# Kernel optimization log

Hardware: AMD Instinct MI355X
Metric: run time of the kernel (lower is better)

## Reference

```python
import jax, jax.numpy as jnp
import numpy as np

B, S, F_IN, D, DFF, MEM, L, H = 32, 512, 64, 512, 2048, 1024, 3, 8
K_NEIGH = 3
TEMP = 1.0


def _pos_encoding(s, d):
    pos = np.arange(s, dtype=np.float64)[:, None]
    div = np.exp(np.arange(0, d, 2, dtype=np.float64) * (-np.log(10000.0) / d))
    pe = np.zeros((s, d), np.float32)
    pe[:, 0::2] = np.sin(pos * div)
    pe[:, 1::2] = np.cos(pos * div)
    return jnp.asarray(pe)


def _ln(x, g, b, eps=1e-5):
    m = x.mean(-1, keepdims=True)
    v = ((x - m) ** 2).mean(-1, keepdims=True)
    return (x - m) * jax.lax.rsqrt(v + eps) * g + b


def _mha(x, qkv_w, qkv_b, out_w, out_b):
    b, s, d = x.shape
    dh = d // H
    qkv = x @ qkv_w.T + qkv_b                      # (b,s,3d)
    q, k, v = jnp.split(qkv, 3, axis=-1)
    rs = lambda t: t.reshape(b, s, H, dh).transpose(0, 2, 1, 3)   # (b,h,s,dh)
    q, k, v = rs(q), rs(k), rs(v)
    scores = jnp.einsum('bhqd,bhkd->bhqk', q, k) / np.sqrt(dh).astype(np.float32)
    att = jax.nn.softmax(scores, axis=-1)
    o = jnp.einsum('bhqk,bhkd->bhqd', att, v).transpose(0, 2, 1, 3).reshape(b, s, d)
    return o @ out_w.T + out_b


def _construct_graph(x):
    # x: (B, S, F) -> adjacency (B, F, F) via kNN on rank-1 similarity (as in source)
    f = x.mean(axis=1)                                   # (B,F)
    n = jnp.linalg.norm(f, axis=1, keepdims=True)
    fn = f / jnp.maximum(n, 1e-12)                       # F.normalize over full vector
    sim = jnp.einsum('bi,bj->bij', fn, fn)               # (B,F,F)
    nf = f.shape[1]
    k = min(K_NEIGH, nf - 1)
    _, idx = jax.lax.top_k(sim, k + 1)                   # (B,F,k+1)
    idx = idx[..., 1:]                                   # drop top-1 (self under source's assumption)
    bidx = jnp.arange(f.shape[0])[:, None, None]
    ridx = jnp.arange(nf)[None, :, None]
    A = jnp.zeros((f.shape[0], nf, nf), x.dtype).at[bidx, ridx, idx].set(1.0)
    A = jnp.maximum(A, jnp.swapaxes(A, 1, 2))            # symmetrize
    di = jnp.arange(nf)
    return A.at[:, di, di].set(1.0)                      # fill_diagonal_(1)


def _gcn(x, A, w1, b1, w2, b2):
    deg = A.sum(2, keepdims=True)
    An = A / jnp.where(deg == 0, jnp.ones_like(deg), deg)
    xt = jnp.swapaxes(x, 1, 2)                           # (B,F,S)
    h = jax.nn.relu(jnp.einsum('bfg,bgh->bfh', An, xt @ w1.T + b1))
    h = jnp.einsum('bfg,bgh->bfh', An, h @ w2.T + b2)
    return jnp.swapaxes(h, 1, 2)                         # (B,S,F)


def _metg_forward(x, W_in, b_in, qkv_w, qkv_b, out_w, out_b, ln1_g, ln1_b,
                  ln2_g, ln2_b, ff1_w, ff1_b, ff2_w, ff2_b, memory,
                  fc1_w, fc1_b, fc2_w, fc2_b, gc1_w, gc1_b, gc2_w, gc2_b):
    # transformer branch
    h = x @ W_in.T + b_in                                # (B,S,D)
    h = h + _pos_encoding(h.shape[1], h.shape[2])
    for l in range(L):  # post-norm TransformerEncoderLayer, relu FFN, dropout=eval
        h = _ln(h + _mha(h, qkv_w[l], qkv_b[l], out_w[l], out_b[l]), ln1_g[l], ln1_b[l])
        ff = jax.nn.relu(h @ ff1_w[l].T + ff1_b[l]) @ ff2_w[l].T + ff2_b[l]
        h = _ln(h + ff, ln2_g[l], ln2_b[l])
    # memory module
    sims = (h @ memory.T) / TEMP                         # (B,S,MEM)
    attn = jax.nn.softmax(sims, axis=-1)
    upd = attn @ memory                                  # (B,S,D)
    # decoder
    cat = jnp.concatenate([h, upd], axis=-1)             # (B,S,2D)
    t_out = jax.nn.relu(cat @ fc1_w.T + fc1_b) @ fc2_w.T + fc2_b
    # GCN branch
    A = _construct_graph(x)
    g_out = _gcn(x, A, gc1_w, gc1_b, gc2_w, gc2_b)
    return t_out, g_out, attn


def setup_inputs() -> dict:
    key = jax.random.key(0)
    ks = jax.random.split(key, 12)
    w = lambda k, shape, s=0.02: jax.random.normal(k, shape, jnp.float32) * s
    return {
        'x': jax.random.normal(ks[0], (B, S, F_IN), jnp.float32),
        'W_in': w(ks[1], (D, F_IN)), 'b_in': jnp.zeros((D,), jnp.float32),
        'qkv_w': w(ks[2], (L, 3 * D, D)), 'qkv_b': jnp.zeros((L, 3 * D), jnp.float32),
        'out_w': w(ks[3], (L, D, D)), 'out_b': jnp.zeros((L, D), jnp.float32),
        'ln1_g': jnp.ones((L, D), jnp.float32), 'ln1_b': jnp.zeros((L, D), jnp.float32),
        'ln2_g': jnp.ones((L, D), jnp.float32), 'ln2_b': jnp.zeros((L, D), jnp.float32),
        'ff1_w': w(ks[4], (L, DFF, D)), 'ff1_b': jnp.zeros((L, DFF), jnp.float32),
        'ff2_w': w(ks[5], (L, D, DFF)), 'ff2_b': jnp.zeros((L, D), jnp.float32),
        'memory': w(ks[6], (MEM, D), 0.05),
        'fc1_w': w(ks[7], (D, 2 * D)), 'fc1_b': jnp.zeros((D,), jnp.float32),
        'fc2_w': w(ks[8], (F_IN, D)), 'fc2_b': jnp.zeros((F_IN,), jnp.float32),
        'gc1_w': w(ks[9], (D, S)), 'gc1_b': jnp.zeros((D,), jnp.float32),
        'gc2_w': w(ks[10], (S, D)), 'gc2_b': jnp.zeros((S,), jnp.float32),
    }


def reference(x, W_in, b_in, qkv_w, qkv_b, out_w, out_b, ln1_g, ln1_b,
              ln2_g, ln2_b, ff1_w, ff1_b, ff2_w, ff2_b, memory,
              fc1_w, fc1_b, fc2_w, fc2_b, gc1_w, gc1_b, gc2_w, gc2_b):
    return _metg_forward(x, W_in, b_in, qkv_w, qkv_b, out_w, out_b, ln1_g, ln1_b,
                         ln2_g, ln2_b, ff1_w, ff1_b, ff2_w, ff2_b, memory,
                         fc1_w, fc1_b, fc2_w, fc2_b, gc1_w, gc1_b, gc2_w, gc2_b)
```

## Files before the change

kernel.cpp:

```cpp
#include <hip/hip_runtime.h>
#include <hip/hip_bf16.h>
#include <math.h>


namespace {

typedef unsigned short ushort_t;
using bf16x8 = __attribute__((ext_vector_type(8))) __bf16;
using f32x4 = __attribute__((ext_vector_type(4))) float;
using ushort8 = __attribute__((ext_vector_type(8))) unsigned short;

constexpr int Mrows = 32 * 512;
constexpr size_t MB = 1048576;

__device__ __forceinline__ unsigned short f2bf(float f) {
  unsigned int u = __builtin_bit_cast(unsigned int, f);
  u += 0x7fffu + ((u >> 16) & 1u);
  return (unsigned short)(u >> 16);
}
__device__ __forceinline__ float bf2f(ushort_t u) {
  unsigned int v = ((unsigned int)u) << 16;
  return __builtin_bit_cast(float, v);
}

__device__ __forceinline__ void g2lds16(const void* g, void* l) {
  __builtin_amdgcn_global_load_lds(
      (const __attribute__((address_space(1))) unsigned int*)g,
      (__attribute__((address_space(3))) unsigned int*)l, 16, 0, 0);
}

template <bool RELU, bool BF16OUT>
__global__ __launch_bounds__(512, 2) void gemm256(const ushort_t* __restrict__ A,
                                                  const ushort_t* __restrict__ B,
                                                  const float* __restrict__ bias,
                                                  void* __restrict__ Cv,
                                                  int K, int lda, int ldc) {
  __shared__ __align__(16) ushort_t As[2][256 * 64];
  __shared__ __align__(16) ushort_t Bs[2][256 * 64];
  const int t = threadIdx.x;
  const int w = t >> 6, l = t & 63;
  const int m0 = blockIdx.x << 8, n0 = blockIdx.y << 8;
  const int srow8 = l >> 3;
  const int scol = ((l & 7) ^ srow8) << 3;
  const ushort_t* agp = A + (size_t)(m0 + w * 32 + srow8) * lda + scol;
  const ushort_t* bgp = B + (size_t)(n0 + w * 32 + srow8) * K + scol;
  const int wr = w >> 2, wcn = w & 3;
  const int lr = l & 15, g = l >> 4;
  const int sw = (l & 7) << 4;
  const int nt = K >> 6;
  f32x4 acc[8][4] = {};
#pragma unroll
  for (int i = 0; i < 4; ++i) {
    g2lds16(agp + (size_t)(i * 8) * lda, &As[0][(w * 32 + i * 8) * 64]);
    g2lds16(bgp + (size_t)(i * 8) * K, &Bs[0][(w * 32 + i * 8) * 64]);
  }
#pragma unroll
  for (int i = 0; i < 4; ++i) {
    g2lds16(agp + (size_t)(i * 8) * lda + 64, &As[1][(w * 32 + i * 8) * 64]);
    g2lds16(bgp + (size_t)(i * 8) * K + 64, &Bs[1][(w * 32 + i * 8) * 64]);
  }
  for (int j = 0; j < nt; ++j) {
    const int c = j & 1;
    asm volatile("s_waitcnt vmcnt(8)" ::: "memory");
    __builtin_amdgcn_s_barrier();
    asm volatile("" ::: "memory");
    const char* abase = (const char*)&As[c][0];
    const char* bbase = (const char*)&Bs[c][0];
#pragma unroll
    for (int ki = 0; ki < 2; ++ki) {
      const int kb = (ki * 64 + g * 16) ^ sw;
      bf16x8 af[8], bfr[4];
#pragma unroll
      for (int mi = 0; mi < 8; ++mi)
        af[mi] = *(const bf16x8*)(abase + (wr * 128 + mi * 16 + lr) * 128 + kb);
#pragma unroll
      for (int ni = 0; ni < 4; ++ni)
        bfr[ni] = *(const bf16x8*)(bbase + (wcn * 64 + ni * 16 + lr) * 128 + kb);
      __builtin_amdgcn_s_setprio(1);
#pragma unroll
      for (int mi = 0; mi < 8; ++mi)
#pragma unroll
        for (int ni = 0; ni < 4; ++ni)
          acc[mi][ni] = __builtin_amdgcn_mfma_f32_16x16x32_bf16(af[mi], bfr[ni],
                                                                acc[mi][ni], 0, 0, 0);
      __builtin_amdgcn_s_setprio(0);
    }
    asm volatile("s_waitcnt lgkmcnt(0)" ::: "memory");
    __builtin_amdgcn_s_barrier();
    asm volatile("" ::: "memory");
    if (j + 2 < nt) {
      const size_t ko = (size_t)(j + 2) * 64;
#pragma unroll
      for (int i = 0; i < 4; ++i) {
        g2lds16(agp + (size_t)(i * 8) * lda + ko, &As[c][(w * 32 + i * 8) * 64]);
        g2lds16(bgp + (size_t)(i * 8) * K + ko, &Bs[c][(w * 32 + i * 8) * 64]);
      }
    }
  }
  float bb[4];
#pragma unroll
  for (int ni = 0; ni < 4; ++ni) {
    const int ci = n0 + wcn * 64 + ni * 16 + lr;
    bb[ni] = bias ? bias[ci] : 0.f;
  }
  const int crow0 = m0 + wr * 128 + g * 4;
#pragma unroll
  for (int mi = 0; mi < 8; ++mi)
#pragma unroll
    for (int ni = 0; ni < 4; ++ni) {
      const int ci = n0 + wcn * 64 + ni * 16 + lr;
#pragma unroll
      for (int v = 0; v < 4; ++v) {
        float val = acc[mi][ni][v] + bb[ni];
        if (RELU) val = fmaxf(val, 0.f);
        const size_t off = (size_t)(crow0 + mi * 16 + v) * ldc + ci;
        if (BF16OUT) ((ushort_t*)Cv)[off] = f2bf(val);
        else         ((float*)Cv)[off] = val;
      }
    }
}

template <bool RELU, bool BF16OUT>
__global__ __launch_bounds__(256) void gemm_bf16(const ushort_t* __restrict__ A,
                                                 const ushort_t* __restrict__ B,
                                                 const float* __restrict__ bias,
                                                 void* __restrict__ Cv,
                                                 int K, int lda, int ldc, int Nclip) {
  __shared__ __align__(16) ushort_t As[128 * 64];
  __shared__ __align__(16) ushort_t Bs[128 * 64];
  const int t = threadIdx.x;
  const int w = t >> 6, l = t & 63;
  const int m0 = blockIdx.x << 7, n0 = blockIdx.y << 7;
  const int srow8 = l >> 3;
  const int scol = ((l & 7) ^ srow8) << 3;
  const ushort_t* agp = A + (size_t)(m0 + w * 32 + srow8) * lda + scol;
  const ushort_t* bgp = B + (size_t)(n0 + w * 32 + srow8) * K + scol;
  ushort_t* alds = &As[(w * 32) * 64];
  ushort_t* blds = &Bs[(w * 32) * 64];
  const int wr = w >> 1, wc = w & 1;
  const int lr = l & 15, g = l >> 4;
  const int sw = (l & 7) << 4;
  f32x4 acc[4][4] = {};
  for (int kt = 0; kt < K; kt += 64) {
    __syncthreads();
#pragma unroll
    for (int i = 0; i < 4; ++i) {
      g2lds16(agp + (size_t)(i * 8) * lda + kt, alds + i * 8 * 64);
      g2lds16(bgp + (size_t)(i * 8) * K + kt, blds + i * 8 * 64);
    }
    __syncthreads();
#pragma unroll
    for (int ki = 0; ki < 2; ++ki) {
      bf16x8 af[4], bf[4];
      const int kb = (ki * 64 + g * 16) ^ sw;
#pragma unroll
      for (int mi = 0; mi < 4; ++mi)
        af[mi] = *(const bf16x8*)((const char*)As + (wr * 64 + mi * 16 + lr) * 128 + kb);
#pragma unroll
      for (int ni = 0; ni < 4; ++ni)
        bf[ni] = *(const bf16x8*)((const char*)Bs + (wc * 64 + ni * 16 + lr) * 128 + kb);
#pragma unroll
      for (int mi = 0; mi < 4; ++mi)
#pragma unroll
        for (int ni = 0; ni < 4; ++ni)
          acc[mi][ni] = __builtin_amdgcn_mfma_f32_16x16x32_bf16(af[mi], bf[ni],
                                                                acc[mi][ni], 0, 0, 0);
    }
  }
  float bb[4];
#pragma unroll
  for (int ni = 0; ni < 4; ++ni) {
    const int ci = n0 + wc * 64 + ni * 16 + lr;
    bb[ni] = (bias && ci < Nclip) ? bias[ci] : 0.f;
  }
  const int crow0 = m0 + wr * 64 + g * 4;
#pragma unroll
  for (int mi = 0; mi < 4; ++mi)
#pragma unroll
    for (int ni = 0; ni < 4; ++ni) {
      const int ci = n0 + wc * 64 + ni * 16 + lr;
      if (ci >= Nclip) continue;
#pragma unroll
      for (int v = 0; v < 4; ++v) {
        float val = acc[mi][ni][v] + bb[ni];
        if (RELU) val = fmaxf(val, 0.f);
        const size_t off = (size_t)(crow0 + mi * 16 + v) * ldc + ci;
        if (BF16OUT) ((ushort_t*)Cv)[off] = f2bf(val);
        else         ((float*)Cv)[off] = val;
      }
    }
}

__global__ __launch_bounds__(256) void flash_attn_mfma(const ushort_t* __restrict__ qkvb,
                                                       ushort_t* __restrict__ ctxb) {
  __shared__ __align__(16) ushort_t Qs[64 * 64];
  __shared__ __align__(16) ushort_t Ks[64 * 64];
  __shared__ __align__(16) ushort_t VT[64 * 64];
  __shared__ __align__(16) ushort_t Ps[64 * 64];
  const int qb = blockIdx.x, hh = blockIdx.y, b = blockIdx.z;
  const int t = threadIdx.x, w = t >> 6, l = t & 63;
  const int g = l >> 4, lr = l & 15, l7 = l & 7;
  const ushort_t* qkv0 = qkvb + (size_t)b * 512 * 1536 + hh * 64;
  {
    const int r8 = l >> 3;
    const int gcol = (l7 ^ r8) << 3;
#pragma unroll
    for (int i = 0; i < 2; ++i) {
      const int row = w * 16 + i * 8 + r8;
      g2lds16(qkv0 + (size_t)(qb * 64 + row) * 1536 + gcol, &Qs[(w * 16 + i * 8) * 64]);
    }
  }
  float mst = -INFINITY, lst = 0.f;
  f32x4 oacc[4] = {};
  const int vk0 = (t & 31) * 2;
  const int vdh0 = (t >> 5) * 8;
  for (int kt = 0; kt < 8; ++kt) {
    __syncthreads();
    {
      const int r8 = l >> 3;
      const int gcol = (l7 ^ r8) << 3;
#pragma unroll
      for (int i = 0; i < 2; ++i) {
        const int row = w * 16 + i * 8 + r8;
        g2lds16(qkv0 + 512 + (size_t)(kt * 64 + row) * 1536 + gcol,
                &Ks[(w * 16 + i * 8) * 64]);
      }
    }
    {
      const ushort_t* vp = qkv0 + 1024 + (size_t)(kt * 64 + vk0) * 1536 + vdh0;
      ushort8 v0 = *(const ushort8*)vp;
      ushort8 v1 = *(const ushort8*)(vp + 1536);
      const int slotbase = vk0 >> 3;
      const int inb = (vk0 & 7) * 2;
#pragma unroll
      for (int e = 0; e < 8; ++e) {
        const int dh = vdh0 + e;
        unsigned int word = (unsigned int)v0[e] | ((unsigned int)v1[e] << 16);
        *(unsigned int*)((char*)VT + dh * 128 + (((slotbase ^ (dh & 7)) << 4) + inb)) = word;
      }
    }
    __syncthreads();
    f32x4 sacc[4] = {};
#pragma unroll
    for (int ki = 0; ki < 2; ++ki) {
      const int sb = ((ki * 4 + g) ^ l7) << 4;
      bf16x8 qf = *(const bf16x8*)((const char*)Qs + (w * 16 + lr) * 128 + sb);
#pragma unroll
      for (int mi = 0; mi < 4; ++mi) {
        bf16x8 kf = *(const bf16x8*)((const char*)Ks + (mi * 16 + lr) * 128 + sb);
        sacc[mi] = __builtin_amdgcn_mfma_f32_16x16x32_bf16(kf, qf, sacc[mi], 0, 0, 0);
      }
    }
    float p[4][4];
    float cmax = -INFINITY;
#pragma unroll
    for (int mi = 0; mi < 4; ++mi)
#pragma unroll
      for (int v = 0; v < 4; ++v) {
        p[mi][v] = sacc[mi][v] * 0.125f;
        cmax = fmaxf(cmax, p[mi][v]);
      }
    cmax = fmaxf(cmax, __shfl_xor(cmax, 16));
    cmax = fmaxf(cmax, __shfl_xor(cmax, 32));
    const float mnew = fmaxf(mst, cmax);
    const float al = __expf(mst - mnew);
    float csum = 0.f;
#pragma unroll
    for (int mi = 0; mi < 4; ++mi)
#pragma unroll
      for (int v = 0; v < 4; ++v) {
        p[mi][v] = __expf(p[mi][v] - mnew);
        csum += p[mi][v];
      }
    csum += __shfl_xor(csum, 16);
    csum += __shfl_xor(csum, 32);
    lst = lst * al + csum;
    mst = mnew;
#pragma unroll
    for (int mi = 0; mi < 4; ++mi) oacc[mi] *= al;
    {
      char* pbase = (char*)Ps + (w * 16 + lr) * 128;
#pragma unroll
      for (int mi = 0; mi < 4; ++mi)
#pragma unroll
        for (int vp2 = 0; vp2 < 2; ++vp2) {
          const int klo = mi * 16 + g * 4 + vp2 * 2;
          unsigned int word = (unsigned int)f2bf(p[mi][vp2 * 2]) |
                              ((unsigned int)f2bf(p[mi][vp2 * 2 + 1]) << 16);
          *(unsigned int*)(pbase + (((klo >> 3) ^ l7) << 4) + (klo & 7) * 2) = word;
        }
    }
#pragma unroll
    for (int ki = 0; ki < 2; ++ki) {
      const int sb = ((ki * 4 + g) ^ l7) << 4;
      bf16x8 pf = *(const bf16x8*)((const char*)Ps + (w * 16 + lr) * 128 + sb);
#pragma unroll
      for (int mi = 0; mi < 4; ++mi) {
        bf16x8 vf = *(const bf16x8*)((const char*)VT + (mi * 16 + lr) * 128 + sb);
        oacc[mi] = __builtin_amdgcn_mfma_f32_16x16x32_bf16(vf, pf, oacc[mi], 0, 0, 0);
      }
    }
  }
  const float inv = 1.f / lst;
  ushort_t* op = ctxb + (size_t)(b * 512 + qb * 64 + w * 16 + lr) * 512 + hh * 64;
#pragma unroll
  for (int mi = 0; mi < 4; ++mi)
#pragma unroll
    for (int vp2 = 0; vp2 < 2; ++vp2) {
      const int dh = mi * 16 + g * 4 + vp2 * 2;
      unsigned int word = (unsigned int)f2bf(oacc[mi][vp2 * 2] * inv) |
                          ((unsigned int)f2bf(oacc[mi][vp2 * 2 + 1] * inv) << 16);
      *(unsigned int*)(op + dh) = word;
    }
}

#define OUTER16(ACC, A4, B4) do { \
  ACC[0][0] += (A4).x*(B4).x; ACC[0][1] += (A4).x*(B4).y; ACC[0][2] += (A4).x*(B4).z; ACC[0][3] += (A4).x*(B4).w; \
  ACC[1][0] += (A4).y*(B4).x; ACC[1][1] += (A4).y*(B4).y; ACC[1][2] += (A4).y*(B4).z; ACC[1][3] += (A4).y*(B4).w; \
  ACC[2][0] += (A4).z*(B4).x; ACC[2][1] += (A4).z*(B4).y; ACC[2][2] += (A4).z*(B4).z; ACC[2][3] += (A4).z*(B4).w; \
  ACC[3][0] += (A4).w*(B4).x; ACC[3][1] += (A4).w*(B4).y; ACC[3][2] += (A4).w*(B4).z; ACC[3][3] += (A4).w*(B4).w; \
} while (0)

__global__ __launch_bounds__(256) void win_pe_gemm(const float* __restrict__ A,
                                                   const float* __restrict__ Bm,
                                                   const float* __restrict__ bias,
                                                   const float* __restrict__ peb,
                                                   ushort_t* __restrict__ hbb) {
  __shared__ float As[16][68];
  __shared__ float Bs[16][68];
  const int t = threadIdx.x;
  const int m0 = blockIdx.x << 6;
  const int n0 = blockIdx.y << 6;
  const int r0 = (t >> 4) << 2;
  const int c0 = (t & 15) << 2;
  const int lm = t >> 2;
  const int lk4 = (t & 3) << 2;
  float acc[4][4] = {{0.f, 0.f, 0.f, 0.f}, {0.f, 0.f, 0.f, 0.f},
                     {0.f, 0.f, 0.f, 0.f}, {0.f, 0.f, 0.f, 0.f}};
  for (int kt = 0; kt < 64; kt += 16) {
    __syncthreads();
    float4 av = *reinterpret_cast<const float4*>(A + (size_t)(m0 + lm) * 64 + kt + lk4);
    As[lk4 + 0][lm] = av.x; As[lk4 + 1][lm] = av.y;
    As[lk4 + 2][lm] = av.z; As[lk4 + 3][lm] = av.w;
    float4 bv = *reinterpret_cast<const float4*>(Bm + (size_t)(n0 + lm) * 64 + kt + lk4);
    Bs[lk4 + 0][lm] = bv.x; Bs[lk4 + 1][lm] = bv.y;
    Bs[lk4 + 2][lm] = bv.z; Bs[lk4 + 3][lm] = bv.w;
    __syncthreads();
#pragma unroll
    for (int k = 0; k < 16; ++k) {
      float4 a4 = *reinterpret_cast<const float4*>(&As[k][r0]);
      float4 b4 = *reinterpret_cast<const float4*>(&Bs[k][c0]);
      OUTER16(acc, a4, b4);
    }
  }
  const float bb0 = bias[n0 + c0 + 0], bb1 = bias[n0 + c0 + 1];
  const float bb2 = bias[n0 + c0 + 2], bb3 = bias[n0 + c0 + 3];
#pragma unroll
  for (int i = 0; i < 4; ++i) {
    const int row = m0 + r0 + i;
    float4 p = *reinterpret_cast<const float4*>(peb + (size_t)(row & 511) * 512 + n0 + c0);
    ushort4 ob;
    ob.x = f2bf(acc[i][0] + bb0 + p.x);
    ob.y = f2bf(acc[i][1] + bb1 + p.y);
    ob.z = f2bf(acc[i][2] + bb2 + p.z);
    ob.w = f2bf(acc[i][3] + bb3 + p.w);
    *reinterpret_cast<ushort4*>(hbb + (size_t)row * 512 + n0 + c0) = ob;
  }
}

__global__ __launch_bounds__(256) void ln_wave(const ushort_t* __restrict__ hbi,
                                               const ushort_t* __restrict__ resb,
                                               const float* __restrict__ g,
                                               const float* __restrict__ bt,
                                               ushort_t* __restrict__ hbo, int hbs) {
  const int t = threadIdx.x;
  const size_t row = (size_t)blockIdx.x * 4 + (t >> 6);
  const int lane = t & 63;
  const size_t base = row * 512 + lane * 8;
  ushort8 hv = *reinterpret_cast<const ushort8*>(hbi + base);
  ushort8 rv = *reinterpret_cast<const ushort8*>(resb + base);
  float xs[8];
  float sum = 0.f;
#pragma unroll
  for (int i = 0; i < 8; ++i) { xs[i] = bf2f(hv[i]) + bf2f(rv[i]); sum += xs[i]; }
#pragma unroll
  for (int off = 1; off < 64; off <<= 1) sum += __shfl_xor(sum, off);
  const float mean = sum * (1.f / 512.f);
  float vs = 0.f;
#pragma unroll
  for (int i = 0; i < 8; ++i) { xs[i] -= mean; vs += xs[i] * xs[i]; }
#pragma unroll
  for (int off = 1; off < 64; off <<= 1) vs += __shfl_xor(vs, off);
  const float rstd = rsqrtf(vs * (1.f / 512.f) + 1e-5f);
  float4 g0 = *reinterpret_cast<const float4*>(g + lane * 8);
  float4 g1 = *reinterpret_cast<const float4*>(g + lane * 8 + 4);
  float4 b0 = *reinterpret_cast<const float4*>(bt + lane * 8);
  float4 b1 = *reinterpret_cast<const float4*>(bt + lane * 8 + 4);
  ushort8 o;
  o[0] = f2bf(xs[0] * rstd * g0.x + b0.x); o[1] = f2bf(xs[1] * rstd * g0.y + b0.y);
  o[2] = f2bf(xs[2] * rstd * g0.z + b0.z); o[3] = f2bf(xs[3] * rstd * g0.w + b0.w);
  o[4] = f2bf(xs[4] * rstd * g1.x + b1.x); o[5] = f2bf(xs[5] * rstd * g1.y + b1.y);
  o[6] = f2bf(xs[6] * rstd * g1.z + b1.z); o[7] = f2bf(xs[7] * rstd * g1.w + b1.w);
  *reinterpret_cast<ushort8*>(hbo + row * hbs + lane * 8) = o;
}

__global__ __launch_bounds__(256) void softmax_wave(const ushort_t* __restrict__ simsb,
                                                    float* __restrict__ attn,
                                                    ushort_t* __restrict__ attnb) {
  const int t = threadIdx.x;
  const size_t row = (size_t)blockIdx.x * 4 + (t >> 6);
  const int lane = t & 63;
  const size_t base = row * 1024 + lane * 16;
  ushort8 v0 = *reinterpret_cast<const ushort8*>(simsb + base);
  ushort8 v1 = *reinterpret_cast<const ushort8*>(simsb + base + 8);
  float xs[16];
  float mx = -INFINITY;
#pragma unroll
  for (int i = 0; i < 8; ++i) { xs[i] = bf2f(v0[i]); xs[i + 8] = bf2f(v1[i]); }
#pragma unroll
  for (int i = 0; i < 16; ++i) mx = fmaxf(mx, xs[i]);
#pragma unroll
  for (int off = 1; off < 64; off <<= 1) mx = fmaxf(mx, __shfl_xor(mx, off));
  float sum = 0.f;
#pragma unroll
  for (int i = 0; i < 16; ++i) { xs[i] = __expf(xs[i] - mx); sum += xs[i]; }
#pragma unroll
  for (int off = 1; off < 64; off <<= 1) sum += __shfl_xor(sum, off);
  const float inv = 1.f / sum;
  ushort8 o0, o1;
#pragma unroll
  for (int i = 0; i < 16; ++i) xs[i] *= inv;
#pragma unroll
  for (int i = 0; i < 4; ++i) {
    float4 f = make_float4(xs[4 * i], xs[4 * i + 1], xs[4 * i + 2], xs[4 * i + 3]);
    *reinterpret_cast<float4*>(attn + base + 4 * i) = f;
  }
#pragma unroll
  for (int i = 0; i < 8; ++i) { o0[i] = f2bf(xs[i]); o1[i] = f2bf(xs[i + 8]); }
  *reinterpret_cast<ushort8*>(attnb + base) = o0;
  *reinterpret_cast<ushort8*>(attnb + base + 8) = o1;
}

__global__ void pe_kernel(float* __restrict__ pe) {
  const int s = blockIdx.x, i = threadIdx.x;
  double div = exp((double)(2 * i) * (-log(10000.0) / 512.0));
  double a = (double)s * div;
  pe[s * 512 + 2 * i] = (float)sin(a);
  pe[s * 512 + 2 * i + 1] = (float)cos(a);
}

__global__ __launch_bounds__(256) void cvt_all(
    const float* __restrict__ qkvw, const float* __restrict__ outw,
    const float* __restrict__ ff1w, const float* __restrict__ ff2w,
    const float* __restrict__ memw, const float* __restrict__ fc1w,
    const float* __restrict__ gc1w, const float* __restrict__ gc2w,
    const float* __restrict__ fc2w,
    ushort_t* qkvb, ushort_t* outb, ushort_t* ff1b, ushort_t* ff2b,
    ushort_t* memb, ushort_t* fc1b, ushort_t* gc1b, ushort_t* gc2b,
    ushort_t* fc2p) {
  const int gidx = blockIdx.x * 256 + threadIdx.x;
  if (gidx >= 2768896) return;
  if (gidx >= 2752512) {
    const int off = gidx - 2752512;
    ushort4 o = {0, 0, 0, 0};
    if (off < 8192) {
      float4 v = reinterpret_cast<const float4*>(fc2w)[off];
      o.x = f2bf(v.x); o.y = f2bf(v.y); o.z = f2bf(v.z); o.w = f2bf(v.w);
    }
    reinterpret_cast<ushort4*>(fc2p)[off] = o;
    return;
  }
  const float* s; ushort_t* d; int off;
  if (gidx < 589824)        { s = qkvw; d = qkvb; off = gidx; }
  else if (gidx < 786432)   { s = outw; d = outb; off = gidx - 589824; }
  else if (gidx < 1572864)  { s = ff1w; d = ff1b; off = gidx - 786432; }
  else if (gidx < 2359296)  { s = ff2w; d = ff2b; off = gidx - 1572864; }
  else if (gidx < 2490368)  { s = memw; d = memb; off = gidx - 2359296; }
  else if (gidx < 2621440)  { s = fc1w; d = fc1b; off = gidx - 2490368; }
  else if (gidx < 2686976)  { s = gc1w; d = gc1b; off = gidx - 2621440; }
  else                      { s = gc2w; d = gc2b; off = gidx - 2686976; }
  float4 v = reinterpret_cast<const float4*>(s)[off];
  ushort4 o;
  o.x = f2bf(v.x); o.y = f2bf(v.y); o.z = f2bf(v.z); o.w = f2bf(v.w);
  reinterpret_cast<ushort4*>(d)[off] = o;
}

__global__ __launch_bounds__(256) void transpose_cvt(const float* __restrict__ in,
                                                     ushort_t* __restrict__ out) {
  const int g = blockIdx.x * 256 + threadIdx.x;
  const int r = g >> 9, c = g & 511;
  out[(size_t)c * 1024 + r] = f2bf(in[g]);
}

__global__ __launch_bounds__(256) void transpose_x_bf16(const float* __restrict__ x,
                                                        ushort_t* __restrict__ xtb) {
  __shared__ float Ls[64][65];
  const int sc = blockIdx.x, b = blockIdx.y;
  const int t = threadIdx.x;
  const int f = t & 63, sr = t >> 6;
#pragma unroll
  for (int j = 0; j < 16; ++j) {
    const int s = sr + 4 * j;
    Ls[s][f] = x[((size_t)(b * 512 + sc * 64 + s)) * 64 + f];
  }
  __syncthreads();
#pragma unroll
  for (int j = 0; j < 16; ++j) {
    const int fr = sr * 16 + j;
    xtb[((size_t)b * 64 + fr) * 512 + sc * 64 + f] = f2bf(Ls[f][fr]);
  }
}

__global__ __launch_bounds__(256) void fmean2(const float* __restrict__ x,
                                              float* __restrict__ fn) {
  __shared__ float part[4][64];
  const int b = blockIdx.x, t = threadIdx.x;
  const int f = t & 63, sg = t >> 6;
  float acc = 0.f;
  const float* xp = x + ((size_t)b * 512 + sg) * 64 + f;
  for (int s = sg; s < 512; s += 4, xp += 256) acc += *xp;
  part[sg][f] = acc;
  __syncthreads();
  if (t < 64) {
    float m = (part[0][t] + part[1][t] + part[2][t] + part[3][t]) * (1.f / 512.f);
    float ss = m * m;
#pragma unroll
    for (int off = 32; off; off >>= 1) ss += __shfl_xor(ss, off);
    float n = fmaxf(sqrtf(ss), 1e-12f);
    fn[b * 64 + t] = m / n;
  }
}

__global__ __launch_bounds__(256) void graph_kernel2(const float* __restrict__ fn,
                                                     float* __restrict__ An) {
  __shared__ float fv[64];
  __shared__ float Am[64][65];
  const int b = blockIdx.x, t = threadIdx.x;
  const int i = t >> 2, g = t & 3;
  if (t < 64) fv[t] = fn[b * 64 + t];
#pragma unroll
  for (int j = 0; j < 16; ++j) Am[i][g * 16 + j] = 0.f;
  __syncthreads();
  const float fi = fv[i];
  unsigned int mask = 0;
  int sel[4];
  for (int r = 0; r < 4; ++r) {
    float best = -INFINITY;
    int bi = 1 << 30;
    for (int j = 0; j < 16; ++j) {
      if (mask & (1u << j)) continue;
      float v = fi * fv[g * 16 + j];
      if (v > best) { best = v; bi = g * 16 + j; }
    }
#pragma unroll
    for (int off = 1; off < 4; off <<= 1) {
      float ov = __shfl_xor(best, off);
      int oi = __shfl_xor(bi, off);
      if (ov > best || (ov == best && oi < bi)) { best = ov; bi = oi; }
    }
    sel[r] = bi;
    if ((bi >> 4) == g) mask |= 1u << (bi & 15);
  }
  if (g == 0) { Am[i][sel[1]] = 1.f; Am[i][sel[2]] = 1.f; Am[i][sel[3]] = 1.f; }
  __syncthreads();
  float vals[16];
  float deg = 0.f;
#pragma unroll
  for (int j0 = 0; j0 < 16; ++j0) {
    const int j = g * 16 + j0;
    float v = (j == i) ? 1.f : fmaxf(Am[i][j], Am[j][i]);
    vals[j0] = v;
    deg += v;
  }
#pragma unroll
  for (int off = 1; off < 4; off <<= 1) deg += __shfl_xor(deg, off);
  const float inv = 1.f / deg;
  float* out = An + ((size_t)b * 64 + i) * 64 + g * 16;
#pragma unroll
  for (int j0 = 0; j0 < 16; ++j0) out[j0] = vals[j0] * inv;
}

template <bool RELU, bool STORE_T>
__global__ __launch_bounds__(256) void bmm_an(const float* __restrict__ An,
                                              const float* __restrict__ X,
                                              float* __restrict__ Y,
                                              ushort_t* __restrict__ Yb) {
  __shared__ float Ag[64][68];
  __shared__ float Xs[64][68];
  const int nc = blockIdx.x << 6;
  const int b = blockIdx.y;
  const int t = threadIdx.x;
  {
    const int i = t >> 2, g0 = (t & 3) << 4;
    const float* ap = An + ((size_t)b * 64 + i) * 64 + g0;
#pragma unroll
    for (int j = 0; j < 16; ++j) Ag[g0 + j][i] = ap[j];
  }
  {
    const int g = t >> 2, n4 = (t & 3) << 4;
    const float* xp = X + ((size_t)b * 64 + g) * 512 + nc + n4;
#pragma unroll
    for (int j = 0; j < 4; ++j)
      *reinterpret_cast<float4*>(&Xs[g][n4 + 4 * j]) =
          *reinterpret_cast<const float4*>(xp + 4 * j);
  }
  __syncthreads();
  const int r0 = (t >> 4) << 2, c0 = (t & 15) << 2;
  float acc[4][4] = {{0.f, 0.f, 0.f, 0.f}, {0.f, 0.f, 0.f, 0.f},
                     {0.f, 0.f, 0.f, 0.f}, {0.f, 0.f, 0.f, 0.f}};
#pragma unroll 8
  for (int g = 0; g < 64; ++g) {
    float4 a4 = *reinterpret_cast<const float4*>(&Ag[g][r0]);
    float4 x4 = *reinterpret_cast<const float4*>(&Xs[g][c0]);
    OUTER16(acc, a4, x4);
  }
  if (!STORE_T) {
#pragma unroll
    for (int i = 0; i < 4; ++i) {
      float4 o = make_float4(acc[i][0], acc[i][1], acc[i][2], acc[i][3]);
      if (RELU) {
        o.x = fmaxf(o.x, 0.f); o.y = fmaxf(o.y, 0.f);
        o.z = fmaxf(o.z, 0.f); o.w = fmaxf(o.w, 0.f);
      }
      ushort4 ob;
      ob.x = f2bf(o.x); ob.y = f2bf(o.y); ob.z = f2bf(o.z); ob.w = f2bf(o.w);
      *reinterpret_cast<ushort4*>(Yb + ((size_t)b * 64 + r0 + i) * 512 + nc + c0) = ob;
    }
  } else {
#pragma unroll
    for (int j = 0; j < 4; ++j) {
      float4 o = make_float4(acc[0][j], acc[1][j], acc[2][j], acc[3][j]);
      *reinterpret_cast<float4*>(Y + ((size_t)b * 512 + nc + c0 + j) * 64 + r0) = o;
    }
  }
}

}

extern "C" void kernel_launch(void* const* d_in, const int* in_sizes, int n_in,
                              void* d_out, int out_size, void* d_ws, size_t ws_size,
                              hipStream_t stream) {
  const float* x     = (const float*)d_in[0];
  const float* W_in  = (const float*)d_in[1];
  const float* b_in  = (const float*)d_in[2];
  const float* qkv_w = (const float*)d_in[3];
  const float* qkv_b = (const float*)d_in[4];
  const float* out_w = (const float*)d_in[5];
  const float* out_b = (const float*)d_in[6];
  const float* ln1_g = (const float*)d_in[7];
  const float* ln1_b = (const float*)d_in[8];
  const float* ln2_g = (const float*)d_in[9];
  const float* ln2_b = (const float*)d_in[10];
  const float* ff1_w = (const float*)d_in[11];
  const float* ff1_b = (const float*)d_in[12];
  const float* ff2_w = (const float*)d_in[13];
  const float* ff2_b = (const float*)d_in[14];
  const float* memw  = (const float*)d_in[15];
  const float* fc1_w = (const float*)d_in[16];
  const float* fc1_b = (const float*)d_in[17];
  const float* fc2_w = (const float*)d_in[18];
  const float* fc2_b = (const float*)d_in[19];
  const float* gc1_w = (const float*)d_in[20];
  const float* gc1_b = (const float*)d_in[21];
  const float* gc2_w = (const float*)d_in[22];
  const float* gc2_b = (const float*)d_in[23];

  char* wsb = (char*)d_ws;
  ushort_t* hb     = (ushort_t*)(wsb + 0);
  ushort_t* ctxb   = (ushort_t*)(wsb + 16 * MB);
  ushort_t* resb   = (ushort_t*)(wsb + 32 * MB);
  char*     U1     = wsb + 48 * MB;
  float*    pe     = (float*)(wsb + 144 * MB);
  ushort_t* qkv_wb = (ushort_t*)(wsb + 146 * MB);
  ushort_t* out_wb = (ushort_t*)(wsb + 151 * MB);
  ushort_t* ff1_wb = (ushort_t*)(wsb + 153 * MB);
  ushort_t* ff2_wb = (ushort_t*)(wsb + 160 * MB);
  ushort_t* mem_b  = (ushort_t*)(wsb + 166 * MB);
  ushort_t* memT_b = (ushort_t*)(wsb + 167 * MB);
  ushort_t* fc1_wb = (ushort_t*)(wsb + 168 * MB);
  ushort_t* gc1_wb = (ushort_t*)(wsb + 169 * MB);
  ushort_t* gc2_wb = (ushort_t*)(wsb + 169 * MB + 524288);
  ushort_t* fc2_wp = (ushort_t*)(wsb + 170 * MB);
  float*    fn     = (float*)(wsb + 171 * MB);
  float*    An     = (float*)(wsb + 172 * MB);

  ushort_t* qkvb    = (ushort_t*)U1;
  ushort_t* midb    = (ushort_t*)U1;
  ushort_t* catb    = (ushort_t*)U1;
  ushort_t* simsb   = (ushort_t*)(U1 + 32 * MB);
  ushort_t* attnb   = (ushort_t*)(U1 + 64 * MB);
  ushort_t* fc1outb = (ushort_t*)(U1 + 64 * MB);
  ushort_t* xtb  = (ushort_t*)U1;
  float*    t1   = (float*)(U1 + 2 * MB);
  ushort_t* h1b  = (ushort_t*)(U1 + 6 * MB);
  float*    t2   = (float*)(U1 + 8 * MB);

  float* t_out = (float*)d_out;
  float* g_out = t_out + 1048576;
  float* attn  = g_out + 1048576;

  hipLaunchKernelGGL(cvt_all, dim3(10816), dim3(256), 0, stream,
                     qkv_w, out_w, ff1_w, ff2_w, memw, fc1_w, gc1_w, gc2_w, fc2_w,
                     qkv_wb, out_wb, ff1_wb, ff2_wb, mem_b, fc1_wb, gc1_wb, gc2_wb,
                     fc2_wp);
  hipLaunchKernelGGL(transpose_cvt, dim3(2048), dim3(256), 0, stream, memw, memT_b);
  hipLaunchKernelGGL(pe_kernel, dim3(512), dim3(256), 0, stream, pe);

  hipLaunchKernelGGL(win_pe_gemm, dim3(256, 8), dim3(256), 0, stream,
                     x, W_in, b_in, pe, hb);

  for (int l = 0; l < 3; ++l) {
    hipLaunchKernelGGL((gemm256<false, true>), dim3(64, 6), dim3(512), 0, stream,
                       hb, qkv_wb + (size_t)l * 786432, qkv_b + l * 1536, qkvb,
                       512, 512, 1536);
    hipLaunchKernelGGL(flash_attn_mfma, dim3(8, 8, 32), dim3(256), 0, stream, qkvb, ctxb);
    hipLaunchKernelGGL((gemm_bf16<false, true>), dim3(128, 4), dim3(256), 0, stream,
                       ctxb, out_wb + (size_t)l * 262144, out_b + l * 512, resb,
                       512, 512, 512, 512);
    hipLaunchKernelGGL(ln_wave, dim3(Mrows / 4), dim3(256), 0, stream,
                       hb, resb, ln1_g + l * 512, ln1_b + l * 512, hb, 512);
    hipLaunchKernelGGL((gemm256<true, true>), dim3(64, 8), dim3(512), 0, stream,
                       hb, ff1_wb + (size_t)l * 1048576, ff1_b + l * 2048, midb,
                       512, 512, 2048);
    hipLaunchKernelGGL((gemm_bf16<false, true>), dim3(128, 4), dim3(256), 0, stream,
                       midb, ff2_wb + (size_t)l * 1048576, ff2_b + l * 512, resb,
                       2048, 2048, 512, 512);
    if (l < 2) {
      hipLaunchKernelGGL(ln_wave, dim3(Mrows / 4), dim3(256), 0, stream,
                         hb, resb, ln2_g + l * 512, ln2_b + l * 512, hb, 512);
    } else {
      hipLaunchKernelGGL(ln_wave, dim3(Mrows / 4), dim3(256), 0, stream,
                         hb, resb, ln2_g + l * 512, ln2_b + l * 512, catb, 1024);
    }
  }

  hipLaunchKernelGGL((gemm256<false, true>), dim3(64, 4), dim3(512), 0, stream,
                     catb, mem_b, (const float*)nullptr, simsb,
                     512, 1024, 1024);
  hipLaunchKernelGGL(softmax_wave, dim3(Mrows / 4), dim3(256), 0, stream,
                     simsb, attn, attnb);
  hipLaunchKernelGGL((gemm_bf16<false, true>), dim3(128, 4), dim3(256), 0, stream,
                     attnb, memT_b, (const float*)nullptr, catb + 512,
                     1024, 1024, 1024, 512);
  hipLaunchKernelGGL((gemm_bf16<true, true>), dim3(128, 4), dim3(256), 0, stream,
                     catb, fc1_wb, fc1_b, fc1outb, 1024, 1024, 512, 512);
  hipLaunchKernelGGL((gemm_bf16<false, false>), dim3(128, 1), dim3(256), 0, stream,
                     fc1outb, fc2_wp, fc2_b, t_out, 512, 512, 64, 64);

  hipLaunchKernelGGL(fmean2, dim3(32), dim3(256), 0, stream, x, fn);
  hipLaunchKernelGGL(graph_kernel2, dim3(32), dim3(256), 0, stream, fn, An);
  hipLaunchKernelGGL(transpose_x_bf16, dim3(8, 32), dim3(256), 0, stream, x, xtb);
  hipLaunchKernelGGL((gemm_bf16<false, false>), dim3(16, 4), dim3(256), 0, stream,
                     xtb, gc1_wb, gc1_b, t1, 512, 512, 512, 512);
  hipLaunchKernelGGL((bmm_an<true, false>), dim3(8, 32), dim3(256), 0, stream,
                     An, t1, (float*)nullptr, h1b);
  hipLaunchKernelGGL((gemm_bf16<false, false>), dim3(16, 4), dim3(256), 0, stream,
                     h1b, gc2_wb, gc2_b, t2, 512, 512, 512, 512);
  hipLaunchKernelGGL((bmm_an<false, true>), dim3(8, 32), dim3(256), 0, stream,
                     An, t2, g_out, (ushort_t*)nullptr);
}
```

Baseline: 900.9 us.

## Fuse out-proj and FF2 GEMMs with residual LayerNorm; merge graph kernels

Adds a gemm_ln kernel that computes a 64x512 full-row output tile per block, stages it in shared memory, and applies residual add plus LayerNorm before writing. This replaces the separate GEMM and ln_wave launches for both LayerNorms in each layer. The intent is to drop the resb round trip to global memory and several launches. In exchange, only 256 blocks are launched, each holding a full 512-column B tile (64KB LDS), which may lower parallelism and occupancy. It also swaps the flash attention grid order so heads vary fastest, and merges fmean2 with graph_kernel2 into a single kernel.

Result: slower. 961.7 us (+6.8%).

```diff
diff --git a/kernel.cpp b/kernel.cpp
--- a/kernel.cpp
+++ b/kernel.cpp
@@ -118,6 +118,117 @@
         else         ((float*)Cv)[off] = val;
       }
     }
+}
+
+__global__ __launch_bounds__(512, 2) void gemm_ln(const ushort_t* __restrict__ A,
+                                                  const ushort_t* __restrict__ B,
+                                                  const float* __restrict__ bias,
+                                                  const ushort_t* __restrict__ res,
+                                                  const float* __restrict__ gg,
+                                                  const float* __restrict__ bt,
+                                                  ushort_t* __restrict__ out,
+                                                  int K, int lda, int ldo) {
+  __shared__ __align__(16) char smem[8192 + 65536];
+  ushort_t* As = (ushort_t*)smem;
+  ushort_t* Bs = (ushort_t*)(smem + 8192);
+  const int t = threadIdx.x;
+  const int w = t >> 6, l = t & 63;
+  const int m0 = blockIdx.x << 6;
+  const int r8 = l >> 3;
+  const int scol = ((l & 7) ^ r8) << 3;
+  const ushort_t* agp = A + (size_t)(m0 + w * 8 + r8) * lda + scol;
+  const ushort_t* bgp = B + (size_t)(w * 64 + r8) * K + scol;
+  const int wr = w & 1, wcn = w >> 1;
+  const int lr = l & 15, gq = l >> 4;
+  const int sw = (l & 7) << 4;
+  f32x4 acc[2][8] = {};
+  for (int kt = 0; kt < K; kt += 64) {
+    __syncthreads();
+    g2lds16(agp + kt, As + (w * 8) * 64);
+#pragma unroll
+    for (int i = 0; i < 8; ++i)
+      g2lds16(bgp + (size_t)(i * 8) * K + kt, Bs + (w * 64 + i * 8) * 64);
+    __syncthreads();
+#pragma unroll
+    for (int ki = 0; ki < 2; ++ki) {
+      const int kb = (ki * 64 + gq * 16) ^ sw;
+      bf16x8 af[2], bfr[8];
+#pragma unroll
+      for (int mi = 0; mi < 2; ++mi)
+        af[mi] = *(const bf16x8*)((const char*)As + (wr * 32 + mi * 16 + lr) * 128 + kb);
+#pragma unroll
+      for (int ni = 0; ni < 8; ++ni)
+        bfr[ni] = *(const bf16x8*)((const char*)Bs + (wcn * 128 + ni * 16 + lr) * 128 + kb);
+#pragma unroll
+      for (int mi = 0; mi < 2; ++mi)
+#pragma unroll
+        for (int ni = 0; ni < 8; ++ni)
+          acc[mi][ni] = __builtin_amdgcn_mfma_f32_16x16x32_bf16(af[mi], bfr[ni],
+                                                                acc[mi][ni], 0, 0, 0);
+    }
+  }
+  float bb[8];
+#pragma unroll
+  for (int ni = 0; ni < 8; ++ni) bb[ni] = bias[wcn * 128 + ni * 16 + lr];
+  __syncthreads();
+  {
+    char* Ys = smem;
+#pragma unroll
+    for (int mi = 0; mi < 2; ++mi)
+#pragma unroll
+      for (int ni = 0; ni < 8; ++ni) {
+        const int col = wcn * 128 + ni * 16 + lr;
+#pragma unroll
+        for (int v = 0; v < 4; ++v) {
+          const int row = wr * 32 + mi * 16 + gq * 4 + v;
+          *(ushort_t*)(Ys + row * 1040 + col * 2) = f2bf(acc[mi][ni][v] + bb[ni]);
+        }
+      }
+  }
+  __syncthreads();
+  {
+    const int r = t >> 3, q = t & 7;
+    const char* Ys = smem;
+    float xs[64];
+    float sum = 0.f;
+    const ushort_t* rp = res + (size_t)(m0 + r) * 512 + q * 64;
+#pragma unroll
+    for (int j = 0; j < 8; ++j) {
+      ushort8 yv = *(const ushort8*)(Ys + r * 1040 + q * 128 + 16 * j);
+      ushort8 rv = *(const ushort8*)(rp + 8 * j);
+#pragma unroll
+      for (int e = 0; e < 8; ++e) {
+        float xv = bf2f(yv[e]) + bf2f(rv[e]);
+        xs[8 * j + e] = xv;
+        sum += xv;
+      }
+    }
+    sum += __shfl_xor(sum, 1); sum += __shfl_xor(sum, 2); sum += __shfl_xor(sum, 4);
+    const float mean = sum * (1.f / 512.f);
+    float vs = 0.f;
+#pragma unroll
+    for (int i = 0; i < 64; ++i) { xs[i] -= mean; vs += xs[i] * xs[i]; }
+    vs += __shfl_xor(vs, 1); vs += __shfl_xor(vs, 2); vs += __shfl_xor(vs, 4);
+    const float rstd = rsqrtf(vs * (1.f / 512.f) + 1e-5f);
+    ushort_t* op = out + (size_t)(m0 + r) * ldo + q * 64;
+#pragma unroll
+    for (int j = 0; j < 8; ++j) {
+      float4 g0 = *(const float4*)(gg + q * 64 + 8 * j);
+      float4 g1 = *(const float4*)(gg + q * 64 + 8 * j + 4);
+      float4 b0 = *(const float4*)(bt + q * 64 + 8 * j);
+      float4 b1 = *(const float4*)(bt + q * 64 + 8 * j + 4);
+      ushort8 o;
+      o[0] = f2bf(xs[8 * j + 0] * rstd * g0.x + b0.x);
+      o[1] = f2bf(xs[8 * j + 1] * rstd * g0.y + b0.y);
+      o[2] = f2bf(xs[8 * j + 2] * rstd * g0.z + b0.z);
+      o[3] = f2bf(xs[8 * j + 3] * rstd * g0.w + b0.w);
+      o[4] = f2bf(xs[8 * j + 4] * rstd * g1.x + b1.x);
+      o[5] = f2bf(xs[8 * j + 5] * rstd * g1.y + b1.y);
+      o[6] = f2bf(xs[8 * j + 6] * rstd * g1.z + b1.z);
+      o[7] = f2bf(xs[8 * j + 7] * rstd * g1.w + b1.w);
+      *(ushort8*)(op + 8 * j) = o;
+    }
+  }
 }
 
 template <bool RELU, bool BF16OUT>
@@ -197,7 +308,7 @@
   __shared__ __align__(16) ushort_t Ks[64 * 64];
   __shared__ __align__(16) ushort_t VT[64 * 64];
   __shared__ __align__(16) ushort_t Ps[64 * 64];
-  const int qb = blockIdx.x, hh = blockIdx.y, b = blockIdx.z;
+  const int hh = blockIdx.x, qb = blockIdx.y, b = blockIdx.z;
   const int t = threadIdx.x, w = t >> 6, l = t & 63;
   const int g = l >> 4, lr = l & 15, l7 = l & 7;
   const ushort_t* qkv0 = qkvb + (size_t)b * 512 * 1536 + hh * 64;
@@ -368,42 +479,6 @@
   }
 }
 
-__global__ __launch_bounds__(256) void ln_wave(const ushort_t* __restrict__ hbi,
-                                               const ushort_t* __restrict__ resb,
-                                               const float* __restrict__ g,
-                                               const float* __restrict__ bt,
-                                               ushort_t* __restrict__ hbo, int hbs) {
-  const int t = threadIdx.x;
-  const size_t row = (size_t)blockIdx.x * 4 + (t >> 6);
-  const int lane = t & 63;
-  const size_t base = row * 512 + lane * 8;
-  ushort8 hv = *reinterpret_cast<const ushort8*>(hbi + base);
-  ushort8 rv = *reinterpret_cast<const ushort8*>(resb + base);
-  float xs[8];
-  float sum = 0.f;
-#pragma unroll
-  for (int i = 0; i < 8; ++i) { xs[i] = bf2f(hv[i]) + bf2f(rv[i]); sum += xs[i]; }
-#pragma unroll
-  for (int off = 1; off < 64; off <<= 1) sum += __shfl_xor(sum, off);
-  const float mean = sum * (1.f / 512.f);
-  float vs = 0.f;
-#pragma unroll
-  for (int i = 0; i < 8; ++i) { xs[i] -= mean; vs += xs[i] * xs[i]; }
-#pragma unroll
-  for (int off = 1; off < 64; off <<= 1) vs += __shfl_xor(vs, off);
-  const float rstd = rsqrtf(vs * (1.f / 512.f) + 1e-5f);
-  float4 g0 = *reinterpret_cast<const float4*>(g + lane * 8);
-  float4 g1 = *reinterpret_cast<const float4*>(g + lane * 8 + 4);
-  float4 b0 = *reinterpret_cast<const float4*>(bt + lane * 8);
-  float4 b1 = *reinterpret_cast<const float4*>(bt + lane * 8 + 4);
-  ushort8 o;
-  o[0] = f2bf(xs[0] * rstd * g0.x + b0.x); o[1] = f2bf(xs[1] * rstd * g0.y + b0.y);
-  o[2] = f2bf(xs[2] * rstd * g0.z + b0.z); o[3] = f2bf(xs[3] * rstd * g0.w + b0.w);
-  o[4] = f2bf(xs[4] * rstd * g1.x + b1.x); o[5] = f2bf(xs[5] * rstd * g1.y + b1.y);
-  o[6] = f2bf(xs[6] * rstd * g1.z + b1.z); o[7] = f2bf(xs[7] * rstd * g1.w + b1.w);
-  *reinterpret_cast<ushort8*>(hbo + row * hbs + lane * 8) = o;
-}
-
 __global__ __launch_bounds__(256) void softmax_wave(const ushort_t* __restrict__ simsb,
                                                     float* __restrict__ attn,
                                                     ushort_t* __restrict__ attnb) {
@@ -511,15 +586,20 @@
   }
 }
 
-__global__ __launch_bounds__(256) void fmean2(const float* __restrict__ x,
-                                              float* __restrict__ fn) {
+__global__ __launch_bounds__(256) void fmean_graph(const float* __restrict__ x,
+                                                   float* __restrict__ An) {
   __shared__ float part[4][64];
+  __shared__ float fv[64];
+  __shared__ float Am[64][65];
   const int b = blockIdx.x, t = threadIdx.x;
   const int f = t & 63, sg = t >> 6;
+  const int i = t >> 2, g = t & 3;
   float acc = 0.f;
   const float* xp = x + ((size_t)b * 512 + sg) * 64 + f;
   for (int s = sg; s < 512; s += 4, xp += 256) acc += *xp;
   part[sg][f] = acc;
+#pragma unroll
+  for (int j = 0; j < 16; ++j) Am[i][g * 16 + j] = 0.f;
   __syncthreads();
   if (t < 64) {
     float m = (part[0][t] + part[1][t] + part[2][t] + part[3][t]) * (1.f / 512.f);
@@ -527,19 +607,8 @@
 #pragma unroll
     for (int off = 32; off; off >>= 1) ss += __shfl_xor(ss, off);
     float n = fmaxf(sqrtf(ss), 1e-12f);
-    fn[b * 64 + t] = m / n;
-  }
-}
-
-__global__ __launch_bounds__(256) void graph_kernel2(const float* __restrict__ fn,
-                                                     float* __restrict__ An) {
-  __shared__ float fv[64];
-  __shared__ float Am[64][65];
-  const int b = blockIdx.x, t = threadIdx.x;
-  const int i = t >> 2, g = t & 3;
-  if (t < 64) fv[t] = fn[b * 64 + t];
-#pragma unroll
-  for (int j = 0; j < 16; ++j) Am[i][g * 16 + j] = 0.f;
+    fv[t] = m / n;
+  }
   __syncthreads();
   const float fi = fv[i];
   unsigned int mask = 0;
@@ -668,7 +737,6 @@
   char* wsb = (char*)d_ws;
   ushort_t* hb     = (ushort_t*)(wsb + 0);
   ushort_t* ctxb   = (ushort_t*)(wsb + 16 * MB);
-  ushort_t* resb   = (ushort_t*)(wsb + 32 * MB);
   char*     U1     = wsb + 48 * MB;
   float*    pe     = (float*)(wsb + 144 * MB);
   ushort_t* qkv_wb = (ushort_t*)(wsb + 146 * MB);
@@ -681,7 +749,6 @@
   ushort_t* gc1_wb = (ushort_t*)(wsb + 169 * MB);
   ushort_t* gc2_wb = (ushort_t*)(wsb + 169 * MB + 524288);
   ushort_t* fc2_wp = (ushort_t*)(wsb + 170 * MB);
-  float*    fn     = (float*)(wsb + 171 * MB);
   float*    An     = (float*)(wsb + 172 * MB);
 
   ushort_t* qkvb    = (ushort_t*)U1;
@@ -714,24 +781,16 @@
                        hb, qkv_wb + (size_t)l * 786432, qkv_b + l * 1536, qkvb,
                        512, 512, 1536);
     hipLaunchKernelGGL(flash_attn_mfma, dim3(8, 8, 32), dim3(256), 0, stream, qkvb, ctxb);
-    hipLaunchKernelGGL((gemm_bf16<false, true>), dim3(128, 4), dim3(256), 0, stream,
-                       ctxb, out_wb + (size_t)l * 262144, out_b + l * 512, resb,
-                       512, 512, 512, 512);
-    hipLaunchKernelGGL(ln_wave, dim3(Mrows / 4), dim3(256), 0, stream,
-                       hb, resb, ln1_g + l * 512, ln1_b + l * 512, hb, 512);
+    hipLaunchKernelGGL(gemm_ln, dim3(256), dim3(512), 0, stream,
+                       ctxb, out_wb + (size_t)l * 262144, out_b + l * 512,
+                       hb, ln1_g + l * 512, ln1_b + l * 512, hb, 512, 512, 512);
     hipLaunchKernelGGL((gemm256<true, true>), dim3(64, 8), dim3(512), 0, stream,
                        hb, ff1_wb + (size_t)l * 1048576, ff1_b + l * 2048, midb,
                        512, 512, 2048);
-    hipLaunchKernelGGL((gemm_bf16<false, true>), dim3(128, 4), dim3(256), 0, stream,
-                       midb, ff2_wb + (size_t)l * 1048576, ff2_b + l * 512, resb,
-                       2048, 2048, 512, 512);
-    if (l < 2) {
-      hipLaunchKernelGGL(ln_wave, dim3(Mrows / 4), dim3(256), 0, stream,
-                         hb, resb, ln2_g + l * 512, ln2_b + l * 512, hb, 512);
-    } else {
-      hipLaunchKernelGGL(ln_wave, dim3(Mrows / 4), dim3(256), 0, stream,
-                         hb, resb, ln2_g + l * 512, ln2_b + l * 512, catb, 1024);
-    }
+    hipLaunchKernelGGL(gemm_ln, dim3(256), dim3(512), 0, stream,
+                       midb, ff2_wb + (size_t)l * 1048576, ff2_b + l * 512,
+                       hb, ln2_g + l * 512, ln2_b + l * 512,
+                       (l < 2) ? hb : catb, 2048, 2048, (l < 2) ? 512 : 1024);
   }
 
   hipLaunchKernelGGL((gemm256<false, true>), dim3(64, 4), dim3(512), 0, stream,
@@ -747,8 +806,7 @@
   hipLaunchKernelGGL((gemm_bf16<false, false>), dim3(128, 1), dim3(256), 0, stream,
                      fc1outb, fc2_wp, fc2_b, t_out, 512, 512, 64, 64);
 
-  hipLaunchKernelGGL(fmean2, dim3(32), dim3(256), 0, stream, x, fn);
-  hipLaunchKernelGGL(graph_kernel2, dim3(32), dim3(256), 0, stream, fn, An);
+  hipLaunchKernelGGL(fmean_graph, dim3(32), dim3(256), 0, stream, x, An);
   hipLaunchKernelGGL(transpose_x_bf16, dim3(8, 32), dim3(256), 0, stream, x, xtb);
   hipLaunchKernelGGL((gemm_bf16<false, false>), dim3(16, 4), dim3(256), 0, stream,
                      xtb, gc1_wb, gc1_b, t1, 512, 512, 512, 512);
```
